# Kernel optimization log

Hardware: AMD Instinct MI355X
Metric: run time of the kernel (lower is better)

Reference implementation:

```python
import jax, jax.numpy as jnp
import numpy as np

NUM_HEADS = 16
HEAD_DIM = 128  # d_out / num_heads = 2048 / 16
WINDOW = 2048   # sliding_window_size


def setup_inputs() -> dict:
    key = jax.random.key(0)
    kx, kq, kk, kv, ko = jax.random.split(key, 5)
    b, s, d = 2, 2048, 2048
    scale = 0.02
    return {
        "x": jax.random.normal(kx, (b, s, d), dtype=jnp.float32),
        "Wq": jax.random.normal(kq, (d, d), dtype=jnp.float32) * scale,
        "Wk": jax.random.normal(kk, (d, d), dtype=jnp.float32) * scale,
        "Wv": jax.random.normal(kv, (d, d), dtype=jnp.float32) * scale,
        "Wo": jax.random.normal(ko, (d, d), dtype=jnp.float32) * scale,
    }


def reference(x, Wq, Wk, Wv, Wo):
    b, s, _ = x.shape
    H, Dh, W = NUM_HEADS, HEAD_DIM, WINDOW

    # qkv projections (no bias), split into heads: [b, s, H, Dh]
    q = (x @ Wq).reshape(b, s, H, Dh)
    k = (x @ Wk).reshape(b, s, H, Dh)
    v = (x @ Wv).reshape(b, s, H, Dh)

    # attn scores: [b, H, q, k]
    scores = jnp.einsum("bqhd,bkhd->bhqk", q, k)

    # sliding-window mask from absolute positions (fresh cache: q_start=k_start=0)
    pos = jnp.arange(s)
    diff = pos[:, None] - pos[None, :]  # q_pos - k_pos
    mask = (diff < 0) | (diff >= W)
    scores = jnp.where(mask[None, None], -jnp.inf, scores)

    attn = jax.nn.softmax(scores / np.sqrt(Dh).astype(np.float32), axis=-1)

    # context: [b, s, H, Dh] -> [b, s, d_out]
    ctx = jnp.einsum("bhqk,bkhd->bqhd", attn, v).reshape(b, s, H * Dh)
    return ctx @ Wo
```

## Files before the change

### kernel.cpp

```cpp
#include <hip/hip_runtime.h>

typedef __bf16 bf16;
typedef __bf16 bf16x4 __attribute__((ext_vector_type(4)));
typedef __bf16 bf16x8 __attribute__((ext_vector_type(8)));
typedef float f32x4 __attribute__((ext_vector_type(4)));

#define B_ 2
#define S_ 2048
#define D_ 2048
#define H_ 16
#define DH_ 128
#define QKVN 6144

__device__ __forceinline__ void async_load16(const bf16* g, bf16* l) {
    __builtin_amdgcn_global_load_lds((const __attribute__((address_space(1))) void*)g,
                                     (__attribute__((address_space(3))) void*)l, 16, 0, 0);
}

__device__ __forceinline__ unsigned int bf16_bits(float x) {
    bf16 h = (bf16)x;
    return (unsigned int)__builtin_bit_cast(unsigned short, h);
}

__global__ __launch_bounds__(256) void cvt_kernel(const float* __restrict__ src,
                                                  bf16* __restrict__ dst) {
    size_t i = (size_t)blockIdx.x * 256 + threadIdx.x;
    const float4* s = (const float4*)src;
    float4 a = s[2 * i], b = s[2 * i + 1];
    bf16x8 o;
    o[0] = (bf16)a.x; o[1] = (bf16)a.y; o[2] = (bf16)a.z; o[3] = (bf16)a.w;
    o[4] = (bf16)b.x; o[5] = (bf16)b.y; o[6] = (bf16)b.z; o[7] = (bf16)b.w;
    *(bf16x8*)(dst + 8 * i) = o;
}

__global__ __launch_bounds__(256) void wtrans_kernel(const float* __restrict__ Wq,
                                                     const float* __restrict__ Wk,
                                                     const float* __restrict__ Wv,
                                                     const float* __restrict__ Wo,
                                                     bf16* __restrict__ WqkvT,
                                                     bf16* __restrict__ WoT) {
    __shared__ unsigned int tile[64][65];
    int z = blockIdx.z;
    const float* src = (z == 0) ? Wq : (z == 1) ? Wk : (z == 2) ? Wv : Wo;
    bf16* dst = (z < 3) ? (WqkvT + (size_t)z * D_ * D_) : WoT;
    int r0 = blockIdx.y * 64, c0 = blockIdx.x * 64;
    int t = threadIdx.x;
    int tr = t >> 4, tc4 = (t & 15) * 4;
#pragma unroll
    for (int it = 0; it < 4; ++it) {
        int r = it * 16 + tr;
        float4 v = *(const float4*)(src + (size_t)(r0 + r) * D_ + c0 + tc4);
        tile[r][tc4 + 0] = bf16_bits(v.x);
        tile[r][tc4 + 1] = bf16_bits(v.y);
        tile[r][tc4 + 2] = bf16_bits(v.z);
        tile[r][tc4 + 3] = bf16_bits(v.w);
    }
    __syncthreads();
#pragma unroll
    for (int it = 0; it < 4; ++it) {
        int a = it * 16 + tr;
        unsigned u0 = tile[tc4 + 0][a], u1 = tile[tc4 + 1][a];
        unsigned u2 = tile[tc4 + 2][a], u3 = tile[tc4 + 3][a];
        uint2 v;
        v.x = (u0 & 0xffffu) | (u1 << 16);
        v.y = (u2 & 0xffffu) | (u3 << 16);
        *(uint2*)(dst + (size_t)(c0 + a) * D_ + r0 + tc4) = v;
    }
}

__global__ __launch_bounds__(256) void vtrans_kernel(const bf16* __restrict__ qkv,
                                                     bf16* __restrict__ vt) {
    __shared__ unsigned int tile[64][65];
    int bh = blockIdx.z;
    int b = bh >> 4, h = bh & 15;
    int s0 = blockIdx.x * 64, d0 = blockIdx.y * 64;
    int t = threadIdx.x, tr = t >> 4, tc4 = (t & 15) * 4;
#pragma unroll
    for (int it = 0; it < 4; ++it) {
        int r = it * 16 + tr;
        uint2 v = *(const uint2*)(qkv + (size_t)(b * S_ + s0 + r) * QKVN + 2 * D_ + h * DH_ + d0 + tc4);
        tile[r][tc4 + 0] = v.x & 0xffffu;
        tile[r][tc4 + 1] = v.x >> 16;
        tile[r][tc4 + 2] = v.y & 0xffffu;
        tile[r][tc4 + 3] = v.y >> 16;
    }
    __syncthreads();
#pragma unroll
    for (int it = 0; it < 4; ++it) {
        int a = it * 16 + tr;
        unsigned u0 = tile[tc4 + 0][a], u1 = tile[tc4 + 1][a];
        unsigned u2 = tile[tc4 + 2][a], u3 = tile[tc4 + 3][a];
        uint2 v;
        v.x = (u0 & 0xffffu) | (u1 << 16);
        v.y = (u2 & 0xffffu) | (u3 << 16);
        *(uint2*)(vt + (size_t)bh * DH_ * S_ + (size_t)(d0 + a) * S_ + s0 + tc4) = v;
    }
}

template <typename CT>
__global__ __launch_bounds__(256) void gemm_bt(const bf16* __restrict__ A,
                                               const bf16* __restrict__ Bt,
                                               CT* __restrict__ C,
                                               int M, int N, int K) {
    __shared__ __align__(16) bf16 As[128 * 32];
    __shared__ __align__(16) bf16 Bs[128 * 32];
    int t = threadIdx.x;
    int w = t >> 6, l = t & 63;
    int quad = l >> 4, lr = l & 15;
    int wr = w >> 1, wc = w & 1;
    size_t m0 = (size_t)blockIdx.y * 128, n0 = (size_t)blockIdx.x * 128;
    int srow = l >> 2, scol = (l & 3) * 8;

    f32x4 acc[4][4];
#pragma unroll
    for (int i = 0; i < 4; ++i)
#pragma unroll
        for (int j = 0; j < 4; ++j) acc[i][j] = (f32x4){0.f, 0.f, 0.f, 0.f};

    for (int k0 = 0; k0 < K; k0 += 32) {
        __syncthreads();
#pragma unroll
        for (int i = 0; i < 2; ++i) {
            int c = w * 2 + i;
            async_load16(A + (m0 + c * 16 + srow) * (size_t)K + k0 + scol, As + c * 512);
            async_load16(Bt + (n0 + c * 16 + srow) * (size_t)K + k0 + scol, Bs + c * 512);
        }
        asm volatile("s_waitcnt vmcnt(0)" ::: "memory");
        __syncthreads();
        bf16x8 af[4], bfr[4];
#pragma unroll
        for (int i = 0; i < 4; ++i) af[i] = *(const bf16x8*)(As + (wr * 64 + i * 16 + lr) * 32 + quad * 8);
#pragma unroll
        for (int j = 0; j < 4; ++j) bfr[j] = *(const bf16x8*)(Bs + (wc * 64 + j * 16 + lr) * 32 + quad * 8);
#pragma unroll
        for (int i = 0; i < 4; ++i)
#pragma unroll
            for (int j = 0; j < 4; ++j)
                acc[i][j] = __builtin_amdgcn_mfma_f32_16x16x32_bf16(af[i], bfr[j], acc[i][j], 0, 0, 0);
    }

    size_t bm = m0 + wr * 64 + quad * 4;
    size_t bn = n0 + wc * 64 + lr;
#pragma unroll
    for (int i = 0; i < 4; ++i)
#pragma unroll
        for (int j = 0; j < 4; ++j)
#pragma unroll
            for (int r = 0; r < 4; ++r)
                C[(bm + i * 16 + r) * (size_t)N + bn + j * 16] = (CT)acc[i][j][r];
}

#define QK_K 2048
#define QK_N 6144

__device__ __forceinline__ bf16x8 lds_frag(const bf16* tile, int row, int colByte) {
    int off = row * 128 + (colByte ^ ((row & 7) << 4));
    return *(const bf16x8*)((const char*)tile + off);
}

template <int MH, int NH>
__device__ __forceinline__ void mmaq8(f32x4 (&acc)[8][4], const bf16x8 (&afr)[4][2],
                                      const bf16x8 (&bf)[2][2]) {
    __builtin_amdgcn_s_setprio(1);
#pragma unroll
    for (int i = 0; i < 4; ++i)
#pragma unroll
        for (int j = 0; j < 2; ++j)
#pragma unroll
            for (int kk = 0; kk < 2; ++kk)
                acc[MH * 4 + i][NH * 2 + j] = __builtin_amdgcn_mfma_f32_16x16x32_bf16(
                    afr[i][kk], bf[j][kk], acc[MH * 4 + i][NH * 2 + j], 0, 0, 0);
    __builtin_amdgcn_s_setprio(0);
}

__global__ __launch_bounds__(512, 2) void gemm_qkv(const bf16* __restrict__ A,
                                                   const bf16* __restrict__ Bt,
                                                   bf16* __restrict__ C) {
    __shared__ __align__(16) bf16 As[2][256 * 64];
    __shared__ __align__(16) bf16 Bs[2][256 * 64];

    int t = threadIdx.x;
    int wid = t >> 6, lane = t & 63;
    int quad = lane >> 4, lr = lane & 15;
    int wr = wid >> 2, wn = wid & 3;

    int bid = blockIdx.x;
    int swz = (bid & 7) * 48 + (bid >> 3);
    int tn = swz >> 4, tm = swz & 15;
    size_t m0 = (size_t)tm * 256, n0 = (size_t)tn * 256;

    int row_r[2], c8s_r[2];
#pragma unroll
    for (int r = 0; r < 2; ++r) {
        int idx = r * 512 + t;
        row_r[r] = idx >> 3;
        c8s_r[r] = (idx & 7) ^ (row_r[r] & 7);
    }

    auto stA = [&](int kt, int bufi, int h) {
#pragma unroll
        for (int r = 0; r < 2; ++r)
            async_load16(A + (m0 + h * 128 + row_r[r]) * (size_t)QK_K + kt * 64 + c8s_r[r] * 8,
                         &As[bufi][(h * 1024 + r * 512 + wid * 64) * 8]);
    };
    auto stB = [&](int kt, int bufi, int h) {
#pragma unroll
        for (int r = 0; r < 2; ++r)
            async_load16(Bt + (n0 + h * 128 + row_r[r]) * (size_t)QK_K + kt * 64 + c8s_r[r] * 8,
                         &Bs[bufi][(h * 1024 + r * 512 + wid * 64) * 8]);
    };

    f32x4 acc[8][4];
#pragma unroll
    for (int i = 0; i < 8; ++i)
#pragma unroll
        for (int j = 0; j < 4; ++j) acc[i][j] = (f32x4){0.f, 0.f, 0.f, 0.f};

    bf16x8 afr[4][2], bf0[2][2], bf1[2][2];

    auto readA = [&](int bufi, int mh) {
#pragma unroll
        for (int i = 0; i < 4; ++i)
#pragma unroll
            for (int kk = 0; kk < 2; ++kk)
                afr[i][kk] = lds_frag(As[bufi], mh * 128 + wr * 64 + i * 16 + lr, kk * 64 + quad * 16);
    };
    auto readB = [&](int bufi, int nh, bf16x8 (&bf)[2][2]) {
#pragma unroll
        for (int j = 0; j < 2; ++j)
#pragma unroll
            for (int kk = 0; kk < 2; ++kk)
                bf[j][kk] = lds_frag(Bs[bufi], nh * 128 + wn * 32 + j * 16 + lr, kk * 64 + quad * 16);
    };

    stA(0, 0, 0); stB(0, 0, 0); stB(0, 0, 1); stA(0, 0, 1);
    asm volatile("s_waitcnt vmcnt(4)" ::: "memory");
    stA(1, 1, 0); stB(1, 1, 0); stB(1, 1, 1);
    asm volatile("s_waitcnt vmcnt(6)" ::: "memory");
    __builtin_amdgcn_s_barrier();

    const int NKT = QK_K / 64;
    for (int it2 = 0; it2 < 15; ++it2) {
        int tt = 2 * it2;
        readA(0, 0);
        readB(0, 0, bf0);
        stA(tt + 1, 1, 1);
        __builtin_amdgcn_s_barrier();
        asm volatile("s_waitcnt lgkmcnt(0)" ::: "memory");
        __builtin_amdgcn_sched_barrier(0);
        mmaq8<0, 0>(acc, afr, bf0);
        __builtin_amdgcn_s_barrier();
        readB(0, 1, bf1);
        stA(tt + 2, 0, 0);
        __builtin_amdgcn_s_barrier();
        asm volatile("s_waitcnt lgkmcnt(0)" ::: "memory");
        __builtin_amdgcn_sched_barrier(0);
        mmaq8<0, 1>(acc, afr, bf1);
        __builtin_amdgcn_s_barrier();
        readA(0, 1);
        stB(tt + 2, 0, 0);
        __builtin_amdgcn_s_barrier();
        asm volatile("s_waitcnt lgkmcnt(0)" ::: "memory");
        __builtin_amdgcn_sched_barrier(0);
        mmaq8<1, 0>(acc, afr, bf0);
        __builtin_amdgcn_s_barrier();
        stB(tt + 2, 0, 1);
        asm volatile("s_waitcnt vmcnt(6)" ::: "memory");
        __builtin_amdgcn_s_barrier();
        mmaq8<1, 1>(acc, afr, bf1);
        __builtin_amdgcn_s_barrier();
        readA(1, 0);
        readB(1, 0, bf0);
        stA(tt + 2, 0, 1);
        __builtin_amdgcn_s_barrier();
        asm volatile("s_waitcnt lgkmcnt(0)" ::: "memory");
        __builtin_amdgcn_sched_barrier(0);
        mmaq8<0, 0>(acc, afr, bf0);
        __builtin_amdgcn_s_barrier();
        readB(1, 1, bf1);
        stA(tt + 3, 1, 0);
        __builtin_amdgcn_s_barrier();
        asm volatile("s_waitcnt lgkmcnt(0)" ::: "memory");
        __builtin_amdgcn_sched_barrier(0);
        mmaq8<0, 1>(acc, afr, bf1);
        __builtin_amdgcn_s_barrier();
        readA(1, 1);
        stB(tt + 3, 1, 0);
        __builtin_amdgcn_s_barrier();
        asm volatile("s_waitcnt lgkmcnt(0)" ::: "memory");
        __builtin_amdgcn_sched_barrier(0);
        mmaq8<1, 0>(acc, afr, bf0);
        __builtin_amdgcn_s_barrier();
        stB(tt + 3, 1, 1);
        asm volatile("s_waitcnt vmcnt(6)" ::: "memory");
        __builtin_amdgcn_s_barrier();
        mmaq8<1, 1>(acc, afr, bf1);
        __builtin_amdgcn_s_barrier();
    }

    {
        readA(0, 0);
        readB(0, 0, bf0);
        stA(31, 1, 1);
        __builtin_amdgcn_s_barrier();
        asm volatile("s_waitcnt lgkmcnt(0)" ::: "memory");
        __builtin_amdgcn_sched_barrier(0);
        mmaq8<0, 0>(acc, afr, bf0);
        __builtin_amdgcn_s_barrier();
        readB(0, 1, bf1);
        __builtin_amdgcn_s_barrier();
        asm volatile("s_waitcnt lgkmcnt(0)" ::: "memory");
        __builtin_amdgcn_sched_barrier(0);
        mmaq8<0, 1>(acc, afr, bf1);
        __builtin_amdgcn_s_barrier();
        readA(0, 1);
        __builtin_amdgcn_s_barrier();
        asm volatile("s_waitcnt lgkmcnt(0)" ::: "memory");
        __builtin_amdgcn_sched_barrier(0);
        mmaq8<1, 0>(acc, afr, bf0);
        __builtin_amdgcn_s_barrier();
        asm volatile("s_waitcnt vmcnt(0)" ::: "memory");
        __builtin_amdgcn_s_barrier();
        mmaq8<1, 1>(acc, afr, bf1);
        __builtin_amdgcn_s_barrier();
        readA(1, 0);
        readB(1, 0, bf0);
        asm volatile("s_waitcnt lgkmcnt(0)" ::: "memory");
        __builtin_amdgcn_sched_barrier(0);
        mmaq8<0, 0>(acc, afr, bf0);
        readB(1, 1, bf1);
        asm volatile("s_waitcnt lgkmcnt(0)" ::: "memory");
        __builtin_amdgcn_sched_barrier(0);
        mmaq8<0, 1>(acc, afr, bf1);
        readA(1, 1);
        asm volatile("s_waitcnt lgkmcnt(0)" ::: "memory");
        __builtin_amdgcn_sched_barrier(0);
        mmaq8<1, 0>(acc, afr, bf0);
        mmaq8<1, 1>(acc, afr, bf1);
    }

#pragma unroll
    for (int mh = 0; mh < 2; ++mh)
#pragma unroll
        for (int i = 0; i < 4; ++i)
#pragma unroll
            for (int nh = 0; nh < 2; ++nh)
#pragma unroll
                for (int j = 0; j < 2; ++j)
#pragma unroll
                    for (int r = 0; r < 4; ++r) {
                        size_t row = m0 + mh * 128 + wr * 64 + i * 16 + quad * 4 + r;
                        size_t col = n0 + nh * 128 + wn * 32 + j * 16 + lr;
                        C[row * QK_N + col] = (bf16)acc[mh * 4 + i][nh * 2 + j][r];
                    }
}

__global__ __launch_bounds__(256, 2) void attn_kernel(const bf16* __restrict__ qkv,
                                                      const bf16* __restrict__ vt,
                                                      bf16* __restrict__ ctx) {
    __shared__ __align__(16) bf16 Ks[2][64 * 128];
    __shared__ __align__(16) bf16 Vts[2][128 * 64];
    __shared__ __align__(16) bf16 Ps[4][16][68];

    int y = blockIdx.y;
    int p = blockIdx.x;
    int b = y >> 4, h = y & 15;
    int t = threadIdx.x, w = t >> 6, l = t & 63;
    int quad = l >> 4, lr = l & 15;

    const bf16* qbase = qkv + (size_t)b * S_ * QKVN + h * DH_;
    const bf16* kbase = qbase + D_;
    const bf16* vbase = vt + (size_t)y * DH_ * S_;

    const int qtA = p, qtB = 31 - p;
    const int nA = p + 1;

    auto stage = [&](int kt, int bi) {
#pragma unroll
        for (int ii = 0; ii < 4; ++ii) {
            int i = 4 * w + ii;
            int row = 4 * i + (l >> 4);
            int cl = (l & 15) ^ (row & 7);
            async_load16(kbase + (size_t)(kt * 64 + row) * QKVN + cl * 8, Ks[bi] + i * 512);
        }
#pragma unroll
        for (int ii = 0; ii < 4; ++ii) {
            int i = 4 * w + ii;
            int dh = 8 * i + (l >> 3);
            int cl = (l & 7) ^ (dh & 7);
            async_load16(vbase + (size_t)dh * S_ + kt * 64 + cl * 8, Vts[bi] + i * 512);
        }
    };

    const float sc2 = 0.12751745f;

    int qt = qtA, q0 = qt * 64;
    bf16x8 qf[4];
    auto loadQ = [&]() {
#pragma unroll
        for (int kk = 0; kk < 4; ++kk) {
            bf16x8 raw = *(const bf16x8*)(qbase + (size_t)(q0 + w * 16 + lr) * QKVN + kk * 32 + quad * 8);
#pragma unroll
            for (int e = 0; e < 8; ++e) qf[kk][e] = (bf16)((float)raw[e] * sc2);
        }
    };
    loadQ();

    float L_r[4];
    f32x4 o[8];
#pragma unroll
    for (int r = 0; r < 4; ++r) L_r[r] = 0.f;
#pragma unroll
    for (int nt = 0; nt < 8; ++nt) o[nt] = (f32x4){0.f, 0.f, 0.f, 0.f};

    auto epilogue = [&](int q0e) {
#pragma unroll
        for (int d = 1; d < 16; d <<= 1)
#pragma unroll
            for (int r = 0; r < 4; ++r) L_r[r] += __shfl_xor(L_r[r], d, 64);
#pragma unroll
        for (int r = 0; r < 4; ++r) {
            float inv = __builtin_amdgcn_rcpf(L_r[r]);
            int q = q0e + w * 16 + quad * 4 + r;
#pragma unroll
            for (int nt = 0; nt < 8; ++nt)
                ctx[(size_t)(b * S_ + q) * D_ + h * DH_ + nt * 16 + lr] = (bf16)(o[nt][r] * inv);
        }
    };

    stage(0, 0);

    for (int it = 0; it < 33; ++it) {
        int buf = it & 1;
        asm volatile("s_waitcnt vmcnt(0)" ::: "memory");
        __syncthreads();
        if (it + 1 < 33) {
            int nit = it + 1;
            int nkt = (nit < nA) ? nit : (nit - nA);
            stage(nkt, buf ^ 1);
        }
        int kt = (it < nA) ? it : (it - nA);

        f32x4 s[4];
#pragma unroll
        for (int jt = 0; jt < 4; ++jt) s[jt] = (f32x4){0.f, 0.f, 0.f, 0.f};
#pragma unroll
        for (int kk = 0; kk < 4; ++kk)
#pragma unroll
            for (int jt = 0; jt < 4; ++jt) {
                bf16x8 kf = *(const bf16x8*)(Ks[buf] + (jt * 16 + lr) * 128 + ((4 * kk + quad) ^ (lr & 7)) * 8);
                s[jt] = __builtin_amdgcn_mfma_f32_16x16x32_bf16(qf[kk], kf, s[jt], 0, 0, 0);
            }

        bool diag = (kt == qt);
#pragma unroll
        for (int jt = 0; jt < 4; ++jt) {
            int keyi = jt * 16 + lr;
#pragma unroll
            for (int r = 0; r < 4; ++r) {
                float s2 = s[jt][r];
                if (diag && keyi > w * 16 + quad * 4 + r) s2 = -3.0e38f;
                float pv = __builtin_amdgcn_exp2f(s2);
                s[jt][r] = pv;
                L_r[r] += pv;
            }
        }
#pragma unroll
        for (int jt = 0; jt < 4; ++jt)
#pragma unroll
            for (int r = 0; r < 4; ++r)
                Ps[w][quad * 4 + r][jt * 16 + lr] = (bf16)s[jt][r];
        asm volatile("s_waitcnt lgkmcnt(0)" ::: "memory");

#pragma unroll
        for (int ks = 0; ks < 2; ++ks) {
            const bf16* pp = &Ps[w][lr][ks * 32 + quad * 8];
            bf16x4 lo = *(const bf16x4*)pp;
            bf16x4 hi = *(const bf16x4*)(pp + 4);
            bf16x8 pf = __builtin_shufflevector(lo, hi, 0, 1, 2, 3, 4, 5, 6, 7);
#pragma unroll
            for (int nt = 0; nt < 8; ++nt) {
                bf16x8 vf = *(const bf16x8*)(Vts[buf] + (nt * 16 + lr) * 64 + ((4 * ks + quad) ^ (lr & 7)) * 8);
                o[nt] = __builtin_amdgcn_mfma_f32_16x16x32_bf16(pf, vf, o[nt], 0, 0, 0);
            }
        }

        if (it == nA - 1) {
            epilogue(q0);
            qt = qtB;
            q0 = qt * 64;
            loadQ();
#pragma unroll
            for (int r = 0; r < 4; ++r) L_r[r] = 0.f;
#pragma unroll
            for (int nt = 0; nt < 8; ++nt) o[nt] = (f32x4){0.f, 0.f, 0.f, 0.f};
        }
    }

    epilogue(q0);
}

extern "C" void kernel_launch(void* const* d_in, const int* in_sizes, int n_in,
                              void* d_out, int out_size, void* d_ws, size_t ws_size,
                              hipStream_t stream) {
    const float* x  = (const float*)d_in[0];
    const float* Wq = (const float*)d_in[1];
    const float* Wk = (const float*)d_in[2];
    const float* Wv = (const float*)d_in[3];
    const float* Wo = (const float*)d_in[4];
    float* out = (float*)d_out;

    char* ws = (char*)d_ws;
    bf16* WqkvT = (bf16*)(ws);
    bf16* WoT   = (bf16*)(ws + 25165824);
    bf16* qkv   = (bf16*)(ws + 33554432);
    bf16* vt    = (bf16*)(ws + 83886080);
    bf16* ctx   = (bf16*)(ws + 100663296);
    bf16* xb    = (bf16*)(ws + 117440512);

    cvt_kernel<<<4096, 256, 0, stream>>>(x, xb);
    wtrans_kernel<<<dim3(32, 32, 4), 256, 0, stream>>>(Wq, Wk, Wv, Wo, WqkvT, WoT);
    gemm_qkv<<<dim3(384), 512, 0, stream>>>(xb, WqkvT, qkv);
    vtrans_kernel<<<dim3(32, 2, 32), 256, 0, stream>>>(qkv, vt);
    attn_kernel<<<dim3(16, 32), 256, 0, stream>>>(qkv, vt, ctx);
    gemm_bt<float><<<dim3(16, 32), 256, 0, stream>>>(ctx, WoT, out, B_ * S_, D_, D_);
}
```

Before: 401.2 us.

## Shrink QKV GEMM tile to 256x128 with triple-buffered LDS pipeline

Changes the QKV projection GEMM from 256x256 tiles to 256x128 tiles, doubling the grid to 768 blocks, and replaces the double-buffered LDS scheme with a three-stage buffer that prefetches two k-tiles ahead. The main loop becomes a simpler two-phase step per k-tile. The goal is better load balance across CUs (384 blocks fit poorly on the device) and more latency hiding from the deeper prefetch. In exchange, each tile has lower arithmetic intensity, so the A operand is read from global memory twice as often.

After: 393.4 us. About the same (-1.9%).

```diff
diff --git a/kernel.cpp b/kernel.cpp
--- a/kernel.cpp
+++ b/kernel.cpp
@@ -158,9 +158,9 @@
     return *(const bf16x8*)((const char*)tile + off);
 }
 
-template <int MH, int NH>
-__device__ __forceinline__ void mmaq8(f32x4 (&acc)[8][4], const bf16x8 (&afr)[4][2],
-                                      const bf16x8 (&bf)[2][2]) {
+template <int MH>
+__device__ __forceinline__ void mmaq16(f32x4 (&acc)[8][2], const bf16x8 (&afr)[4][2],
+                                       const bf16x8 (&bf)[2][2]) {
     __builtin_amdgcn_s_setprio(1);
 #pragma unroll
     for (int i = 0; i < 4; ++i)
@@ -168,16 +168,16 @@
         for (int j = 0; j < 2; ++j)
 #pragma unroll
             for (int kk = 0; kk < 2; ++kk)
-                acc[MH * 4 + i][NH * 2 + j] = __builtin_amdgcn_mfma_f32_16x16x32_bf16(
-                    afr[i][kk], bf[j][kk], acc[MH * 4 + i][NH * 2 + j], 0, 0, 0);
+                acc[MH * 4 + i][j] = __builtin_amdgcn_mfma_f32_16x16x32_bf16(
+                    afr[i][kk], bf[j][kk], acc[MH * 4 + i][j], 0, 0, 0);
     __builtin_amdgcn_s_setprio(0);
 }
 
 __global__ __launch_bounds__(512, 2) void gemm_qkv(const bf16* __restrict__ A,
                                                    const bf16* __restrict__ Bt,
                                                    bf16* __restrict__ C) {
-    __shared__ __align__(16) bf16 As[2][256 * 64];
-    __shared__ __align__(16) bf16 Bs[2][256 * 64];
+    __shared__ __align__(16) bf16 As[3][256 * 64];
+    __shared__ __align__(16) bf16 Bs[3][128 * 64];
 
     int t = threadIdx.x;
     int wid = t >> 6, lane = t & 63;
@@ -185,9 +185,9 @@
     int wr = wid >> 2, wn = wid & 3;
 
     int bid = blockIdx.x;
-    int swz = (bid & 7) * 48 + (bid >> 3);
+    int swz = (bid & 7) * 96 + (bid >> 3);
     int tn = swz >> 4, tm = swz & 15;
-    size_t m0 = (size_t)tm * 256, n0 = (size_t)tn * 256;
+    size_t m0 = (size_t)tm * 256, n0 = (size_t)tn * 128;
 
     int row_r[2], c8s_r[2];
 #pragma unroll
@@ -203,20 +203,20 @@
             async_load16(A + (m0 + h * 128 + row_r[r]) * (size_t)QK_K + kt * 64 + c8s_r[r] * 8,
                          &As[bufi][(h * 1024 + r * 512 + wid * 64) * 8]);
     };
-    auto stB = [&](int kt, int bufi, int h) {
+    auto stB = [&](int kt, int bufi) {
 #pragma unroll
         for (int r = 0; r < 2; ++r)
-            async_load16(Bt + (n0 + h * 128 + row_r[r]) * (size_t)QK_K + kt * 64 + c8s_r[r] * 8,
-                         &Bs[bufi][(h * 1024 + r * 512 + wid * 64) * 8]);
-    };
-
-    f32x4 acc[8][4];
+            async_load16(Bt + (n0 + row_r[r]) * (size_t)QK_K + kt * 64 + c8s_r[r] * 8,
+                         &Bs[bufi][(r * 512 + wid * 64) * 8]);
+    };
+
+    f32x4 acc[8][2];
 #pragma unroll
     for (int i = 0; i < 8; ++i)
 #pragma unroll
-        for (int j = 0; j < 4; ++j) acc[i][j] = (f32x4){0.f, 0.f, 0.f, 0.f};
-
-    bf16x8 afr[4][2], bf0[2][2], bf1[2][2];
+        for (int j = 0; j < 2; ++j) acc[i][j] = (f32x4){0.f, 0.f, 0.f, 0.f};
+
+    bf16x8 afr[4][2], bf[2][2];
 
     auto readA = [&](int bufi, int mh) {
 #pragma unroll
@@ -225,118 +225,74 @@
             for (int kk = 0; kk < 2; ++kk)
                 afr[i][kk] = lds_frag(As[bufi], mh * 128 + wr * 64 + i * 16 + lr, kk * 64 + quad * 16);
     };
-    auto readB = [&](int bufi, int nh, bf16x8 (&bf)[2][2]) {
+    auto readB = [&](int bufi) {
 #pragma unroll
         for (int j = 0; j < 2; ++j)
 #pragma unroll
             for (int kk = 0; kk < 2; ++kk)
-                bf[j][kk] = lds_frag(Bs[bufi], nh * 128 + wn * 32 + j * 16 + lr, kk * 64 + quad * 16);
-    };
-
-    stA(0, 0, 0); stB(0, 0, 0); stB(0, 0, 1); stA(0, 0, 1);
-    asm volatile("s_waitcnt vmcnt(4)" ::: "memory");
-    stA(1, 1, 0); stB(1, 1, 0); stB(1, 1, 1);
-    asm volatile("s_waitcnt vmcnt(6)" ::: "memory");
+                bf[j][kk] = lds_frag(Bs[bufi], wn * 32 + j * 16 + lr, kk * 64 + quad * 16);
+    };
+
+    stB(0, 0); stA(0, 0, 0); stA(0, 0, 1);
+    stB(1, 1); stA(1, 1, 0); stA(1, 1, 1);
+    asm volatile("s_waitcnt vmcnt(8)" ::: "memory");
     __builtin_amdgcn_s_barrier();
 
-    const int NKT = QK_K / 64;
-    for (int it2 = 0; it2 < 15; ++it2) {
-        int tt = 2 * it2;
-        readA(0, 0);
-        readB(0, 0, bf0);
-        stA(tt + 1, 1, 1);
-        __builtin_amdgcn_s_barrier();
-        asm volatile("s_waitcnt lgkmcnt(0)" ::: "memory");
-        __builtin_amdgcn_sched_barrier(0);
-        mmaq8<0, 0>(acc, afr, bf0);
-        __builtin_amdgcn_s_barrier();
-        readB(0, 1, bf1);
-        stA(tt + 2, 0, 0);
-        __builtin_amdgcn_s_barrier();
-        asm volatile("s_waitcnt lgkmcnt(0)" ::: "memory");
-        __builtin_amdgcn_sched_barrier(0);
-        mmaq8<0, 1>(acc, afr, bf1);
-        __builtin_amdgcn_s_barrier();
-        readA(0, 1);
-        stB(tt + 2, 0, 0);
-        __builtin_amdgcn_s_barrier();
-        asm volatile("s_waitcnt lgkmcnt(0)" ::: "memory");
-        __builtin_amdgcn_sched_barrier(0);
-        mmaq8<1, 0>(acc, afr, bf0);
-        __builtin_amdgcn_s_barrier();
-        stB(tt + 2, 0, 1);
-        asm volatile("s_waitcnt vmcnt(6)" ::: "memory");
-        __builtin_amdgcn_s_barrier();
-        mmaq8<1, 1>(acc, afr, bf1);
-        __builtin_amdgcn_s_barrier();
-        readA(1, 0);
-        readB(1, 0, bf0);
-        stA(tt + 2, 0, 1);
-        __builtin_amdgcn_s_barrier();
-        asm volatile("s_waitcnt lgkmcnt(0)" ::: "memory");
-        __builtin_amdgcn_sched_barrier(0);
-        mmaq8<0, 0>(acc, afr, bf0);
-        __builtin_amdgcn_s_barrier();
-        readB(1, 1, bf1);
-        stA(tt + 3, 1, 0);
-        __builtin_amdgcn_s_barrier();
-        asm volatile("s_waitcnt lgkmcnt(0)" ::: "memory");
-        __builtin_amdgcn_sched_barrier(0);
-        mmaq8<0, 1>(acc, afr, bf1);
-        __builtin_amdgcn_s_barrier();
-        readA(1, 1);
-        stB(tt + 3, 1, 0);
-        __builtin_amdgcn_s_barrier();
-        asm volatile("s_waitcnt lgkmcnt(0)" ::: "memory");
-        __builtin_amdgcn_sched_barrier(0);
-        mmaq8<1, 0>(acc, afr, bf0);
-        __builtin_amdgcn_s_barrier();
-        stB(tt + 3, 1, 1);
-        asm volatile("s_waitcnt vmcnt(6)" ::: "memory");
-        __builtin_amdgcn_s_barrier();
-        mmaq8<1, 1>(acc, afr, bf1);
-        __builtin_amdgcn_s_barrier();
+    auto tile2ph = [&](int kt, int cb, int nb2) {
+        readA(cb, 0);
+        readB(cb);
+        stB(kt + 2, nb2);
+        stA(kt + 2, nb2, 0);
+        __builtin_amdgcn_s_barrier();
+        asm volatile("s_waitcnt lgkmcnt(0)" ::: "memory");
+        __builtin_amdgcn_sched_barrier(0);
+        mmaq16<0>(acc, afr, bf);
+        asm volatile("s_waitcnt vmcnt(10)" ::: "memory");
+        __builtin_amdgcn_s_barrier();
+        readA(cb, 1);
+        stA(kt + 2, nb2, 1);
+        __builtin_amdgcn_s_barrier();
+        asm volatile("s_waitcnt lgkmcnt(0)" ::: "memory");
+        __builtin_amdgcn_sched_barrier(0);
+        mmaq16<1>(acc, afr, bf);
+        asm volatile("s_waitcnt vmcnt(8)" ::: "memory");
+        __builtin_amdgcn_s_barrier();
+    };
+
+    for (int kt3 = 0; kt3 < 30; kt3 += 3) {
+        tile2ph(kt3 + 0, 0, 2);
+        tile2ph(kt3 + 1, 1, 0);
+        tile2ph(kt3 + 2, 2, 1);
     }
 
     {
         readA(0, 0);
-        readB(0, 0, bf0);
-        stA(31, 1, 1);
-        __builtin_amdgcn_s_barrier();
-        asm volatile("s_waitcnt lgkmcnt(0)" ::: "memory");
-        __builtin_amdgcn_sched_barrier(0);
-        mmaq8<0, 0>(acc, afr, bf0);
-        __builtin_amdgcn_s_barrier();
-        readB(0, 1, bf1);
-        __builtin_amdgcn_s_barrier();
-        asm volatile("s_waitcnt lgkmcnt(0)" ::: "memory");
-        __builtin_amdgcn_sched_barrier(0);
-        mmaq8<0, 1>(acc, afr, bf1);
+        readB(0);
+        __builtin_amdgcn_s_barrier();
+        asm volatile("s_waitcnt lgkmcnt(0)" ::: "memory");
+        __builtin_amdgcn_sched_barrier(0);
+        mmaq16<0>(acc, afr, bf);
+        asm volatile("s_waitcnt vmcnt(6)" ::: "memory");
         __builtin_amdgcn_s_barrier();
         readA(0, 1);
         __builtin_amdgcn_s_barrier();
         asm volatile("s_waitcnt lgkmcnt(0)" ::: "memory");
         __builtin_amdgcn_sched_barrier(0);
-        mmaq8<1, 0>(acc, afr, bf0);
-        __builtin_amdgcn_s_barrier();
+        mmaq16<1>(acc, afr, bf);
+        asm volatile("s_waitcnt vmcnt(2)" ::: "memory");
+        __builtin_amdgcn_s_barrier();
+        readA(1, 0);
+        readB(1);
+        __builtin_amdgcn_s_barrier();
+        asm volatile("s_waitcnt lgkmcnt(0)" ::: "memory");
+        __builtin_amdgcn_sched_barrier(0);
+        mmaq16<0>(acc, afr, bf);
         asm volatile("s_waitcnt vmcnt(0)" ::: "memory");
         __builtin_amdgcn_s_barrier();
-        mmaq8<1, 1>(acc, afr, bf1);
-        __builtin_amdgcn_s_barrier();
-        readA(1, 0);
-        readB(1, 0, bf0);
-        asm volatile("s_waitcnt lgkmcnt(0)" ::: "memory");
-        __builtin_amdgcn_sched_barrier(0);
-        mmaq8<0, 0>(acc, afr, bf0);
-        readB(1, 1, bf1);
-        asm volatile("s_waitcnt lgkmcnt(0)" ::: "memory");
-        __builtin_amdgcn_sched_barrier(0);
-        mmaq8<0, 1>(acc, afr, bf1);
         readA(1, 1);
         asm volatile("s_waitcnt lgkmcnt(0)" ::: "memory");
         __builtin_amdgcn_sched_barrier(0);
-        mmaq8<1, 0>(acc, afr, bf0);
-        mmaq8<1, 1>(acc, afr, bf1);
+        mmaq16<1>(acc, afr, bf);
     }
 
 #pragma unroll
@@ -344,15 +300,13 @@
 #pragma unroll
         for (int i = 0; i < 4; ++i)
 #pragma unroll
-            for (int nh = 0; nh < 2; ++nh)
-#pragma unroll
-                for (int j = 0; j < 2; ++j)
-#pragma unroll
-                    for (int r = 0; r < 4; ++r) {
-                        size_t row = m0 + mh * 128 + wr * 64 + i * 16 + quad * 4 + r;
-                        size_t col = n0 + nh * 128 + wn * 32 + j * 16 + lr;
-                        C[row * QK_N + col] = (bf16)acc[mh * 4 + i][nh * 2 + j][r];
-                    }
+            for (int j = 0; j < 2; ++j)
+#pragma unroll
+                for (int r = 0; r < 4; ++r) {
+                    size_t row = m0 + mh * 128 + wr * 64 + i * 16 + quad * 4 + r;
+                    size_t col = n0 + wn * 32 + j * 16 + lr;
+                    C[row * QK_N + col] = (bf16)acc[mh * 4 + i][j][r];
+                }
 }
 
 __global__ __launch_bounds__(256, 2) void attn_kernel(const bf16* __restrict__ qkv,
@@ -520,7 +474,7 @@
 
     cvt_kernel<<<4096, 256, 0, stream>>>(x, xb);
     wtrans_kernel<<<dim3(32, 32, 4), 256, 0, stream>>>(Wq, Wk, Wv, Wo, WqkvT, WoT);
-    gemm_qkv<<<dim3(384), 512, 0, stream>>>(xb, WqkvT, qkv);
+    gemm_qkv<<<dim3(768), 512, 0, stream>>>(xb, WqkvT, qkv);
     vtrans_kernel<<<dim3(32, 2, 32), 256, 0, stream>>>(qkv, vt);
     attn_kernel<<<dim3(16, 32), 256, 0, stream>>>(qkv, vt, ctx);
     gemm_bt<float><<<dim3(16, 32), 256, 0, stream>>>(ctx, WoT, out, B_ * S_, D_, D_);
```
